# Kernel optimization log

Hardware: AMD Instinct MI355X
Metric: run time of the kernel (lower is better)

## Reference

```python
import jax, jax.numpy as jnp
import numpy as np

B, S, D, H = 4, 2048, 1024, 16


def setup_inputs() -> dict:
    key = jax.random.key(0)
    ks = jax.random.split(key, 5)
    scale = 1.0 / np.sqrt(D)
    return {
        "q": jax.random.normal(ks[0], (B, S, D), jnp.float32),
        "v": jax.random.normal(ks[1], (B, S, D), jnp.float32),
        "Wq": jax.random.normal(ks[2], (D, D), jnp.float32) * scale,
        "bq": jnp.zeros((D,), jnp.float32),
        "Wk": jax.random.normal(ks[3], (D, D), jnp.float32) * scale,
        "bk": jnp.zeros((D,), jnp.float32),
        "Wv": jax.random.normal(ks[4], (D, D), jnp.float32) * scale,
        "bv": jnp.zeros((D,), jnp.float32),
    }


def reference(q, v, Wq, bq, Wk, bk, Wv, bv):
    # k defaults to v in the original call
    k = v
    embed_dim = Wq.shape[0]
    num_heads = H
    dh = embed_dim // num_heads
    b, s, _ = q.shape

    qp = q @ Wq + bq  # [B,S,D]
    kp = k @ Wk + bk
    vp = v @ Wv + bv

    # tf.split(x, H, axis=2) + concat on axis 0 == reshape to [B,S,H,dh]
    qh = qp.reshape(b, s, num_heads, dh)
    kh = kp.reshape(b, s, num_heads, dh)
    vh = vp.reshape(b, s, num_heads, dh)

    # NOTE: original scales by sqrt(embed_dim), NOT sqrt(head_dim)
    scores = jnp.einsum("bqhd,bkhd->bhqk", qh, kh) / jnp.sqrt(
        jnp.asarray(embed_dim, qh.dtype)
    )
    att = jax.nn.softmax(scores, axis=-1)
    out = jnp.einsum("bhqk,bkhd->bqhd", att, vh)
    return out.reshape(b, s, embed_dim)
```

## Files before the change

### kernel.cpp

```cpp
#include <hip/hip_runtime.h>
#include <hip/hip_bf16.h>
#include <math.h>

#define B_   4
#define S_   2048
#define D_   1024
#define H_   16
#define DH_  64
#define M_   (B_ * S_)
#define BH_  (B_ * H_)

typedef __bf16 bf16x8_t __attribute__((ext_vector_type(8)));
typedef float  f32x4_t  __attribute__((ext_vector_type(4)));
typedef float  f32x16_t __attribute__((ext_vector_type(16)));

#define QSCALE 0.045084220027780106f

__device__ __forceinline__ unsigned short f2bf(float x) {
  unsigned int u = __float_as_uint(x);
  u += 0x7fffu + ((u >> 16) & 1u);
  return (unsigned short)(u >> 16);
}

__device__ __forceinline__ unsigned int pk2t(float lo, float hi) {
  return __builtin_amdgcn_perm(__float_as_uint(hi), __float_as_uint(lo), 0x07060302u);
}

__device__ __forceinline__ void async16(const void* g, void* l) {
  __builtin_amdgcn_global_load_lds(
      (__attribute__((address_space(1))) unsigned int*)(void*)g,
      (__attribute__((address_space(3))) unsigned int*)l, 16, 0, 0);
}

__global__ __launch_bounds__(256) void cvt_f32_bf16(
    const float* __restrict__ q, const float* __restrict__ v,
    unsigned short* __restrict__ qb, unsigned short* __restrict__ vb) {
  const float* src = blockIdx.y ? v : q;
  unsigned short* dst = blockIdx.y ? vb : qb;
  size_t i = ((size_t)blockIdx.x * 256 + threadIdx.x) * 4;
  float4 a = *(const float4*)(src + i);
  ushort4 o;
  o.x = f2bf(a.x); o.y = f2bf(a.y); o.z = f2bf(a.z); o.w = f2bf(a.w);
  *(ushort4*)(dst + i) = o;
}

__global__ void wtrans(const float* __restrict__ Wq, const float* __restrict__ Wk,
                       const float* __restrict__ Wv,
                       unsigned short* __restrict__ Wqt, unsigned short* __restrict__ Wkt,
                       unsigned short* __restrict__ Wvt) {
  int z = blockIdx.z;
  const float* W = (z == 0) ? Wq : (z == 1 ? Wk : Wv);
  unsigned short* Wt = (z == 0) ? Wqt : (z == 1 ? Wkt : Wvt);
  __shared__ float tile[32][33];
  int tx = threadIdx.x, ty = threadIdx.y;
  int n = blockIdx.x * 32 + tx;
#pragma unroll
  for (int i = 0; i < 4; ++i) {
    int k = blockIdx.y * 32 + ty + i * 8;
    tile[ty + i * 8][tx] = W[(size_t)k * D_ + n];
  }
  __syncthreads();
  int k2 = blockIdx.y * 32 + tx;
#pragma unroll
  for (int i = 0; i < 4; ++i) {
    int n2 = blockIdx.x * 32 + ty + i * 8;
    Wt[(size_t)n2 * D_ + k2] = f2bf(tile[tx][ty + i * 8]);
  }
}

__global__ __launch_bounds__(256) void proj_gemm(
    const unsigned short* __restrict__ Aq, const unsigned short* __restrict__ Av,
    const unsigned short* __restrict__ Wqt, const unsigned short* __restrict__ Wkt,
    const unsigned short* __restrict__ Wvt,
    const float* __restrict__ bq, const float* __restrict__ bk, const float* __restrict__ bv,
    unsigned short* __restrict__ qp, unsigned short* __restrict__ kp,
    unsigned short* __restrict__ vt) {
  int z = blockIdx.y;
  const unsigned short* A  = (z == 0) ? Aq : Av;
  const unsigned short* Wt = (z == 0) ? Wqt : (z == 1 ? Wkt : Wvt);
  const float* bias        = (z == 0) ? bq : (z == 1 ? bk : bv);
  unsigned short* outp     = (z == 0) ? qp : (z == 1 ? kp : vt);
  const float cs           = (z == 0) ? QSCALE : 1.0f;

  int lin = blockIdx.x;
  int xcd = lin & 7, j = lin >> 3;
  int m0 = (xcd * 8 + (j & 7)) * 128;
  int n0 = (j >> 3) * 128;

  __shared__ __attribute__((aligned(16))) unsigned short Alds[128 * 64];
  __shared__ __attribute__((aligned(16))) unsigned short Blds[128 * 64];

  int t = threadIdx.x;
  int lane = t & 63, wave = t >> 6;
  int lrow = lane & 15, lq = lane >> 4;
  int wm = (wave & 1) * 64, wn = (wave >> 1) * 64;

  f32x4_t acc[4][4];
#pragma unroll
  for (int i = 0; i < 4; ++i)
#pragma unroll
    for (int j2 = 0; j2 < 4; ++j2) acc[i][j2] = (f32x4_t){0.f, 0.f, 0.f, 0.f};

  for (int k0 = 0; k0 < D_; k0 += 64) {
    __syncthreads();
#pragma unroll
    for (int r = 0; r < 4; ++r) {
      int off = t * 16 + r * 4096;
      int row = off >> 7, slot = (off >> 4) & 7;
      int ch = slot ^ (row & 7);
      async16((const char*)A  + ((size_t)(m0 + row) * D_ + k0) * 2 + ch * 16, (char*)Alds + off);
      async16((const char*)Wt + ((size_t)(n0 + row) * D_ + k0) * 2 + ch * 16, (char*)Blds + off);
    }
    __syncthreads();

#pragma unroll
    for (int kk = 0; kk < 2; ++kk) {
      bf16x8_t af[4], bfr[4];
#pragma unroll
      for (int i = 0; i < 4; ++i) {
        int ra = wm + i * 16 + lrow;
        int rb = wn + i * 16 + lrow;
        af[i]  = *(const bf16x8_t*)((const char*)Alds + ra * 128 + (((lq + 4 * kk) ^ (ra & 7)) * 16));
        bfr[i] = *(const bf16x8_t*)((const char*)Blds + rb * 128 + (((lq + 4 * kk) ^ (rb & 7)) * 16));
      }
#pragma unroll
      for (int i = 0; i < 4; ++i)
#pragma unroll
        for (int j2 = 0; j2 < 4; ++j2)
          acc[i][j2] = __builtin_amdgcn_mfma_f32_16x16x32_bf16(af[i], bfr[j2], acc[i][j2], 0, 0, 0);
    }
  }

#pragma unroll
  for (int j2 = 0; j2 < 4; ++j2) {
    int n = n0 + wn + j2 * 16 + lrow;
    float bv_ = bias[n];
    int h = n >> 6, d = n & 63;
#pragma unroll
    for (int i = 0; i < 4; ++i) {
      int mbase = m0 + wm + i * 16 + lq * 4;
      int b = mbase >> 11, s = mbase & 2047;
      if (z != 2) {
#pragma unroll
        for (int r = 0; r < 4; ++r)
          outp[(((size_t)(b * H_ + h) * S_ + (s + r)) << 6) + d] = f2bf((acc[i][j2][r] + bv_) * cs);
      } else {
        ushort4 pk;
        pk.x = f2bf(acc[i][j2][0] + bv_);
        pk.y = f2bf(acc[i][j2][1] + bv_);
        pk.z = f2bf(acc[i][j2][2] + bv_);
        pk.w = f2bf(acc[i][j2][3] + bv_);
        *(ushort4*)(outp + (((size_t)(b * H_ + h) * 64 + d) << 11) + s) = pk;
      }
    }
  }
}

__global__ __launch_bounds__(256, 4) void attn(
    const unsigned short* __restrict__ qp, const unsigned short* __restrict__ kp,
    const unsigned short* __restrict__ vt, float* __restrict__ out) {
  const int bh = blockIdx.x;
  const int qt = blockIdx.y;
  const int t = threadIdx.x;
  const int lane = t & 63, wave = t >> 6;
  const int h = lane >> 5, ln = lane & 31;

  __shared__ __attribute__((aligned(16))) unsigned short Klds[2][64 * 64];
  __shared__ __attribute__((aligned(16))) unsigned short Vlds[2][64 * 64];

  const int q0 = qt * 128 + wave * 32;

  bf16x8_t qf[4];
#pragma unroll
  for (int ks = 0; ks < 4; ++ks)
    qf[ks] = *(const bf16x8_t*)(qp + ((size_t)bh * S_ + q0 + ln) * 64 + ks * 16 + h * 8);

  f32x16_t o[2];
  f32x16_t o_l;
#pragma unroll
  for (int r = 0; r < 16; ++r) { o[0][r] = 0.f; o[1][r] = 0.f; o_l[r] = 0.f; }

  f32x16_t z16;
#pragma unroll
  for (int r = 0; r < 16; ++r) z16[r] = 0.f;

  bf16x8_t onesf;
#pragma unroll
  for (int i = 0; i < 8; ++i) onesf[i] = (__bf16)1.0f;

  const unsigned short* kg = kp + (size_t)bh * S_ * 64;
  const unsigned short* vg = vt + (size_t)bh * 64 * S_;

  auto stage = [&](int kb, int bi) {
#pragma unroll
    for (int r = 0; r < 2; ++r) {
      int off = t * 16 + r * 4096;
      int row = off >> 7, slot = (off >> 4) & 7;
      int ch = slot ^ (row & 7);
      async16((const char*)(kg + (size_t)(kb + row) * 64 + ch * 8), (char*)&Klds[bi][0] + off);
      async16((const char*)(vg + (size_t)row * S_ + kb + ch * 8), (char*)&Vlds[bi][0] + off);
    }
  };

  stage(0, 0);

  const int NT = S_ / 64;
  for (int it = 0; it < NT; ++it) {
    const int bi = it & 1;
    __syncthreads();
    if (it + 1 < NT) stage((it + 1) * 64, bi ^ 1);

    const unsigned short* Kb = &Klds[bi][0];
    const unsigned short* Vb = &Vlds[bi][0];

    f32x16_t st[2];
#pragma unroll
    for (int kt = 0; kt < 2; ++kt) {
      int row = kt * 32 + ln;
      {
        bf16x8_t kf = *(const bf16x8_t*)(Kb + row * 64 + ((h ^ (row & 7)) * 8));
        st[kt] = __builtin_amdgcn_mfma_f32_32x32x16_bf16(kf, qf[0], z16, 0, 0, 0);
      }
#pragma unroll
      for (int ks = 1; ks < 4; ++ks) {
        bf16x8_t kf = *(const bf16x8_t*)(Kb + row * 64 + (((ks * 2 + h) ^ (row & 7)) * 8));
        st[kt] = __builtin_amdgcn_mfma_f32_32x32x16_bf16(kf, qf[ks], st[kt], 0, 0, 0);
      }
    }

    unsigned int pkv[2][8];
#pragma unroll
    for (int kt = 0; kt < 2; ++kt)
#pragma unroll
      for (int i = 0; i < 8; ++i) {
        float p0 = __builtin_amdgcn_exp2f(st[kt][2 * i]);
        float p1 = __builtin_amdgcn_exp2f(st[kt][2 * i + 1]);
        pkv[kt][i] = pk2t(p0, p1);
      }

    bf16x8_t pf[4];
#pragma unroll
    for (int ks = 0; ks < 4; ++ks) {
      int kt = ks >> 1, b = 4 * (ks & 1);
      unsigned int e0 = __shfl_xor(h ? pkv[kt][b]     : pkv[kt][b + 2], 32);
      unsigned int e1 = __shfl_xor(h ? pkv[kt][b + 1] : pkv[kt][b + 3], 32);
      union { unsigned int u[4]; bf16x8_t v; } fr;
      fr.u[0] = h ? e0 : pkv[kt][b];
      fr.u[1] = h ? e1 : pkv[kt][b + 1];
      fr.u[2] = h ? pkv[kt][b + 2] : e0;
      fr.u[3] = h ? pkv[kt][b + 3] : e1;
      pf[ks] = fr.v;
    }

#pragma unroll
    for (int ks = 0; ks < 4; ++ks)
      o_l = __builtin_amdgcn_mfma_f32_32x32x16_bf16(pf[ks], onesf, o_l, 0, 0, 0);

#pragma unroll
    for (int dt = 0; dt < 2; ++dt) {
      int row = dt * 32 + ln;
#pragma unroll
      for (int ks = 0; ks < 4; ++ks) {
        bf16x8_t vf = *(const bf16x8_t*)(Vb + row * 64 + (((ks * 2 + h) ^ (row & 7)) * 8));
        o[dt] = __builtin_amdgcn_mfma_f32_32x32x16_bf16(pf[ks], vf, o[dt], 0, 0, 0);
      }
    }
  }

  const int b = bh >> 4, head = bh & 15;
#pragma unroll
  for (int r = 0; r < 16; ++r) {
    int rowl = (r & 3) + 8 * (r >> 2) + 4 * h;
    float inv = __builtin_amdgcn_rcpf(o_l[r]);
    int rg = q0 + rowl;
    float* op = out + ((size_t)b * S_ + rg) * D_ + head * 64 + ln;
    op[0]  = o[0][r] * inv;
    op[32] = o[1][r] * inv;
  }
}

extern "C" void kernel_launch(void* const* d_in, const int* in_sizes, int n_in,
                              void* d_out, int out_size, void* d_ws, size_t ws_size,
                              hipStream_t stream) {
  const float* q  = (const float*)d_in[0];
  const float* v  = (const float*)d_in[1];
  const float* Wq = (const float*)d_in[2];
  const float* bq = (const float*)d_in[3];
  const float* Wk = (const float*)d_in[4];
  const float* bk = (const float*)d_in[5];
  const float* Wv = (const float*)d_in[6];
  const float* bv = (const float*)d_in[7];
  float* out = (float*)d_out;

  char* ws = (char*)d_ws;
  unsigned short* qb  = (unsigned short*)(ws);
  unsigned short* vb  = (unsigned short*)(ws + (16u << 20));
  unsigned short* Wqt = (unsigned short*)(ws + (32u << 20));
  unsigned short* Wkt = (unsigned short*)(ws + (34u << 20));
  unsigned short* Wvt = (unsigned short*)(ws + (36u << 20));
  unsigned short* qpp = (unsigned short*)(ws + (38u << 20));
  unsigned short* kpp = (unsigned short*)(ws + (54u << 20));
  unsigned short* vtp = (unsigned short*)(ws + (70u << 20));

  hipLaunchKernelGGL(cvt_f32_bf16, dim3((M_ * D_) / 1024, 2), dim3(256), 0, stream,
                     q, v, qb, vb);
  hipLaunchKernelGGL(wtrans, dim3(32, 32, 3), dim3(32, 8), 0, stream,
                     Wq, Wk, Wv, Wqt, Wkt, Wvt);
  hipLaunchKernelGGL(proj_gemm, dim3(512, 3), dim3(256), 0, stream,
                     qb, vb, Wqt, Wkt, Wvt, bq, bk, bv, qpp, kpp, vtp);
  hipLaunchKernelGGL(attn, dim3(BH_, S_ / 128), dim3(256), 0, stream,
                     qpp, kpp, vtp, out);
}
```

Before: 279.1 us.

## Load V fragments directly from global, compute row sums in registers

V tiles are no longer staged through LDS. Each wave now reads its V MFMA operands straight from global memory into registers, which halves the shared-memory footprint and the async copy traffic. The softmax denominator is accumulated as a scalar per lane during exponentiation instead of through an extra MFMA against a ones vector, with shuffles at the end to redistribute it. The lane-half exchange uses permlane32_swap when the builtin is available. The risk is that V global loads are repeated by all four waves without LDS sharing, and their latency is exposed.

After: 320.6 us. 1.15x slower.

```diff
diff --git a/kernel.cpp b/kernel.cpp
--- a/kernel.cpp
+++ b/kernel.cpp
@@ -13,6 +13,7 @@
 typedef __bf16 bf16x8_t __attribute__((ext_vector_type(8)));
 typedef float  f32x4_t  __attribute__((ext_vector_type(4)));
 typedef float  f32x16_t __attribute__((ext_vector_type(16)));
+typedef unsigned int uint2v __attribute__((ext_vector_type(2)));
 
 #define QSCALE 0.045084220027780106f
 
@@ -166,7 +167,6 @@
   const int h = lane >> 5, ln = lane & 31;
 
   __shared__ __attribute__((aligned(16))) unsigned short Klds[2][64 * 64];
-  __shared__ __attribute__((aligned(16))) unsigned short Vlds[2][64 * 64];
 
   const int q0 = qt * 128 + wave * 32;
 
@@ -176,20 +176,16 @@
     qf[ks] = *(const bf16x8_t*)(qp + ((size_t)bh * S_ + q0 + ln) * 64 + ks * 16 + h * 8);
 
   f32x16_t o[2];
-  f32x16_t o_l;
-#pragma unroll
-  for (int r = 0; r < 16; ++r) { o[0][r] = 0.f; o[1][r] = 0.f; o_l[r] = 0.f; }
+  float l = 0.f;
+#pragma unroll
+  for (int r = 0; r < 16; ++r) { o[0][r] = 0.f; o[1][r] = 0.f; }
 
   f32x16_t z16;
 #pragma unroll
   for (int r = 0; r < 16; ++r) z16[r] = 0.f;
 
-  bf16x8_t onesf;
-#pragma unroll
-  for (int i = 0; i < 8; ++i) onesf[i] = (__bf16)1.0f;
-
   const unsigned short* kg = kp + (size_t)bh * S_ * 64;
-  const unsigned short* vg = vt + (size_t)bh * 64 * S_;
+  const unsigned short* vg = vt + ((size_t)bh * 64 + ln) * S_ + h * 8;
 
   auto stage = [&](int kb, int bi) {
 #pragma unroll
@@ -198,7 +194,6 @@
       int row = off >> 7, slot = (off >> 4) & 7;
       int ch = slot ^ (row & 7);
       async16((const char*)(kg + (size_t)(kb + row) * 64 + ch * 8), (char*)&Klds[bi][0] + off);
-      async16((const char*)(vg + (size_t)row * S_ + kb + ch * 8), (char*)&Vlds[bi][0] + off);
     }
   };
 
@@ -207,11 +202,16 @@
   const int NT = S_ / 64;
   for (int it = 0; it < NT; ++it) {
     const int bi = it & 1;
+    const int kb = it * 64;
     __syncthreads();
-    if (it + 1 < NT) stage((it + 1) * 64, bi ^ 1);
+    if (it + 1 < NT) stage(kb + 64, bi ^ 1);
+
+    bf16x8_t vf0[4];
+#pragma unroll
+    for (int ks = 0; ks < 4; ++ks)
+      vf0[ks] = *(const bf16x8_t*)(vg + kb + ks * 16);
 
     const unsigned short* Kb = &Klds[bi][0];
-    const unsigned short* Vb = &Vlds[bi][0];
 
     f32x16_t st[2];
 #pragma unroll
@@ -228,50 +228,61 @@
       }
     }
 
+    bf16x8_t vf1[4];
+#pragma unroll
+    for (int ks = 0; ks < 4; ++ks)
+      vf1[ks] = *(const bf16x8_t*)(vg + 32 * S_ + kb + ks * 16);
+
     unsigned int pkv[2][8];
+    float lp = 0.f;
 #pragma unroll
     for (int kt = 0; kt < 2; ++kt)
 #pragma unroll
       for (int i = 0; i < 8; ++i) {
         float p0 = __builtin_amdgcn_exp2f(st[kt][2 * i]);
         float p1 = __builtin_amdgcn_exp2f(st[kt][2 * i + 1]);
+        lp += p0 + p1;
         pkv[kt][i] = pk2t(p0, p1);
       }
+    l += lp;
 
     bf16x8_t pf[4];
 #pragma unroll
     for (int ks = 0; ks < 4; ++ks) {
       int kt = ks >> 1, b = 4 * (ks & 1);
+      union { unsigned int u[4]; bf16x8_t v; } fr;
+#if __has_builtin(__builtin_amdgcn_permlane32_swap)
+      uint2v s02 = __builtin_amdgcn_permlane32_swap(pkv[kt][b],     pkv[kt][b + 2], false, false);
+      uint2v s13 = __builtin_amdgcn_permlane32_swap(pkv[kt][b + 1], pkv[kt][b + 3], false, false);
+      fr.u[0] = s02[0]; fr.u[2] = s02[1];
+      fr.u[1] = s13[0]; fr.u[3] = s13[1];
+#else
       unsigned int e0 = __shfl_xor(h ? pkv[kt][b]     : pkv[kt][b + 2], 32);
       unsigned int e1 = __shfl_xor(h ? pkv[kt][b + 1] : pkv[kt][b + 3], 32);
-      union { unsigned int u[4]; bf16x8_t v; } fr;
       fr.u[0] = h ? e0 : pkv[kt][b];
       fr.u[1] = h ? e1 : pkv[kt][b + 1];
       fr.u[2] = h ? pkv[kt][b + 2] : e0;
       fr.u[3] = h ? pkv[kt][b + 3] : e1;
+#endif
       pf[ks] = fr.v;
     }
 
 #pragma unroll
     for (int ks = 0; ks < 4; ++ks)
-      o_l = __builtin_amdgcn_mfma_f32_32x32x16_bf16(pf[ks], onesf, o_l, 0, 0, 0);
-
-#pragma unroll
-    for (int dt = 0; dt < 2; ++dt) {
-      int row = dt * 32 + ln;
-#pragma unroll
-      for (int ks = 0; ks < 4; ++ks) {
-        bf16x8_t vf = *(const bf16x8_t*)(Vb + row * 64 + (((ks * 2 + h) ^ (row & 7)) * 8));
-        o[dt] = __builtin_amdgcn_mfma_f32_32x32x16_bf16(pf[ks], vf, o[dt], 0, 0, 0);
-      }
-    }
-  }
+      o[0] = __builtin_amdgcn_mfma_f32_32x32x16_bf16(pf[ks], vf0[ks], o[0], 0, 0, 0);
+#pragma unroll
+    for (int ks = 0; ks < 4; ++ks)
+      o[1] = __builtin_amdgcn_mfma_f32_32x32x16_bf16(pf[ks], vf1[ks], o[1], 0, 0, 0);
+  }
+
+  l += __shfl_xor(l, 32);
 
   const int b = bh >> 4, head = bh & 15;
 #pragma unroll
   for (int r = 0; r < 16; ++r) {
     int rowl = (r & 3) + 8 * (r >> 2) + 4 * h;
-    float inv = __builtin_amdgcn_rcpf(o_l[r]);
+    float li = __shfl(l, rowl, 64);
+    float inv = __builtin_amdgcn_rcpf(li);
     int rg = q0 + rowl;
     float* op = out + ((size_t)b * S_ + rg) * D_ + head * 64 + ln;
     op[0]  = o[0][r] * inv;
```
